# Kernel optimization log

Measured on AMD Instinct MI355X. Metric: run time of the kernel, lower is better.

## Reference

```python
import jax, jax.numpy as jnp
import numpy as np

# Multi-scale AvgPool3d pyramid (stride 1, zero padding, count_include_pad=True as in torch)
KERNELS = [(1, 1, 1), (1, 5, 5), (3, 13, 13), (5, 23, 23), (7, 31, 31), (9, 41, 41)]
WEIGHTS = [w / 100.0 for w in [20, 20, 20, 20, 20, 20, 10, 10]]
EPS = 1e-7  # BatchDiceLoss epsilon


def avgpool3d(x, k):
    # x: [B, C, D, H, W]; separable sum-pool per axis then divide by full kernel size
    # (equivalent to torch AvgPool3d with count_include_pad=True, stride 1, pad=(k-1)//2)
    y = x
    for axis, ks in zip((2, 3, 4), k):
        if ks > 1:
            window = [1] * 5
            window[axis] = ks
            pad = [(0, 0)] * 5
            pad[axis] = (ks // 2, ks // 2)
            y = jax.lax.reduce_window(y, 0.0, jax.lax.add, tuple(window), (1,) * 5, tuple(pad))
    return y / float(np.prod(k))


def batch_dice(pred, target):
    # BatchDiceLoss([1.0]): single label channel 0, flattened over the whole batch
    p = pred[:, 0].reshape(-1)
    t = target[:, 0].reshape(-1)
    inter = jnp.sum(p * t)
    return 1.0 - (2.0 * inter) / (jnp.sum(p) + jnp.sum(t) + EPS)


def multi_scale_dc(pred, target):
    loss = 0.0
    for k in KERNELS:
        pp = avgpool3d(avgpool3d(pred, k), k)   # pool applied twice per scale
        tt = avgpool3d(avgpool3d(target, k), k)
        loss = loss + batch_dice(pp, tt)
    return loss / len(KERNELS)


def setup_inputs() -> dict:
    key = jax.random.key(0)
    ks = jax.random.split(key, 14)
    vol = (4, 1, 28, 160, 160)
    u = lambda k: jax.random.uniform(k, vol, dtype=jnp.float32)
    return {
        "pr_core_c": u(ks[0]),
        "pr_core_p": u(ks[1]),
        "gt_core": u(ks[2]),
        "pr_lesion_c": u(ks[3]),
        "pr_lesion_p": u(ks[4]),
        "gt_lesion": u(ks[5]),
        "pr_penu_c": u(ks[6]),
        "pr_penu_p": u(ks[7]),
        "gt_penu": u(ks[8]),
        "output": jax.random.uniform(ks[9], (4, 6, 28, 160, 160), dtype=jnp.float32),
        "off_core_c": jax.random.normal(ks[10], (4, 3), dtype=jnp.float32),
        "off_penu_p": jax.random.normal(ks[11], (4, 3), dtype=jnp.float32),
        "off_target_c": jax.random.normal(ks[12], (4, 3), dtype=jnp.float32),
        "off_target_p": jax.random.normal(ks[13], (4, 3), dtype=jnp.float32),
    }


def reference(pr_core_c, pr_core_p, gt_core, pr_lesion_c, pr_lesion_p, gt_lesion,
              pr_penu_c, pr_penu_p, gt_penu, output,
              off_core_c, off_penu_p, off_target_c, off_target_p):
    loss = WEIGHTS[0] * multi_scale_dc(pr_core_c, gt_core)
    loss += WEIGHTS[1] * multi_scale_dc(pr_core_p, gt_core)
    loss += WEIGHTS[2] * multi_scale_dc(pr_lesion_c, gt_lesion)
    loss += WEIGHTS[3] * multi_scale_dc(pr_lesion_p, gt_lesion)
    loss += WEIGHTS[4] * multi_scale_dc(pr_penu_c, gt_penu)
    loss += WEIGHTS[5] * multi_scale_dc(pr_penu_p, gt_penu)
    # temporal monotonicity penalty: mean(|diff| - diff) per consecutive time pair
    diff = output[:, 1:] - output[:, :-1]           # [B, T-1, D, H, W]
    loss += WEIGHTS[6] * jnp.sum(jnp.mean(jnp.abs(diff) - diff, axis=(0, 2, 3, 4)))
    loss += WEIGHTS[7] * jnp.mean(jnp.abs(off_core_c - off_target_c))
    loss += WEIGHTS[7] * jnp.mean(jnp.abs(off_penu_p - off_target_p))
    return loss
```

## Files before the change

### kernel.cpp

```cpp
#include <hip/hip_runtime.h>
#include <hip/hip_fp16.h>


#define DIMB 4
#define DIMD 28
#define DIMH 160
#define DIMW 160
#define HW   (DIMH * DIMW)
#define DHW  (DIMD * HW)
#define VOL_N (DIMB * DHW)
#define PGRID 640
#define NSLOTS 91
#define DICE_EPS 1e-7
#define TBL_OFF (480 * 1024)

__device__ __forceinline__ float u2f(int pos, int k, int L) {
    if (k == 1) return 1.f;
    int r = k >> 1;
    float s = 0.f;
    for (int j = max(pos - r, 0); j <= min(pos + r, L - 1); ++j)
        s += (float)(min(j + r, L - 1) - max(j - r, 0) + 1);
    return s / (float)(k * k);
}

__device__ __forceinline__ float wave_sum(float v) {
#pragma unroll
    for (int o = 1; o < 64; o <<= 1) v += __shfl_xor(v, o, 64);
    return v;
}

__device__ __forceinline__ __half2 shfl_h2(__half2 v, int src) {
    int x = __shfl(*reinterpret_cast<int*>(&v), src, 64);
    return *reinterpret_cast<__half2*>(&x);
}

template<int K>
__device__ __forceinline__ void hstore(const float (&raw)[40],
                                       unsigned char* __restrict__ ob,
                                       int l, int c, int wl, int h0)
{
    constexpr int R = K / 2;
    constexpr float INVK = 1.f / (float)K;
    float ox[40];
#pragma unroll
    for (int i = 0; i < 40; ++i) ox[i] = raw[i];
#pragma unroll
    for (int pass = 0; pass < 4; ++pass) {
        float lo[R], hi[R];
#pragma unroll
        for (int i = 0; i < R; ++i) {
            float a = __shfl(ox[40 - R + i], l - 16, 64);
            lo[i] = (c == 0) ? 0.f : a;
            float b = __shfl(ox[i], l + 16, 64);
            hi[i] = (c == 3) ? 0.f : b;
        }
#define HWIN(j) ((j) < R ? lo[(j)] : ((j) < R + 40 ? ox[(j) - R] : hi[(j) - R - 40]))
        float out[40];
        float s = 0.f;
#pragma unroll
        for (int j = 0; j <= 2 * R; ++j) s += HWIN(j);
        out[0] = s * INVK;
#pragma unroll
        for (int i = 1; i < 40; ++i) {
            s += HWIN(i + 2 * R) - HWIN(i - 1);
            out[i] = s * INVK;
        }
#undef HWIN
#pragma unroll
        for (int i = 0; i < 40; ++i) ox[i] = out[i];
    }
#pragma unroll
    for (int i = 0; i < 40; ++i)
        ob[(h0 + i) * DIMW + wl] = (unsigned char)__float2uint_rn(ox[i] * 255.f);
}

__global__ __launch_bounds__(256) void hpool_tbl(const float* __restrict__ g0,
    const float* __restrict__ g1, const float* __restrict__ g2,
    unsigned char* __restrict__ bufs, float* __restrict__ tbl)
{
    int bx = blockIdx.x;
    if (bx < 840) {
        int u = bx * 2 + (threadIdx.x >> 7);
        int tt = threadIdx.x & 127;
        int g = u / 560, r = u - g * 560;
        int bd = r / 5, wt = r - bd * 5;
        const float* in = (g == 0) ? g0 : (g == 1) ? g1 : g2;
        int l = tt & 63, v = tt >> 6;
        int c = l >> 4, wl = v * 16 + (l & 15), h0 = c * 40;
        const float* base = in + (size_t)bd * HW + wt * 32;
        float raw[40];
#pragma unroll
        for (int i = 0; i < 40; ++i) raw[i] = base[(h0 + i) * DIMW + wl];
        unsigned char* ob = bufs + (size_t)g * 5 * VOL_N + (size_t)bd * HW + wt * 32;
        hstore<5> (raw, ob + 0 * (size_t)VOL_N, l, c, wl, h0);
        hstore<13>(raw, ob + 1 * (size_t)VOL_N, l, c, wl, h0);
        hstore<23>(raw, ob + 2 * (size_t)VOL_N, l, c, wl, h0);
        hstore<31>(raw, ob + 3 * (size_t)VOL_N, l, c, wl, h0);
        hstore<41>(raw, ob + 4 * (size_t)VOL_N, l, c, wl, h0);
    } else {
        const int KDa[6] = {1, 1, 3, 5, 7, 9};
        const int KHa[6] = {1, 5, 13, 23, 31, 41};
        for (int e = threadIdx.x; e < 1128; e += 256) {
            if (e < 960) tbl[e] = u2f(e % 160, KHa[e / 160], DIMH);
            else {
                int q = e - 960;
                tbl[e] = u2f(q % 28, KDa[q / 28], DIMD);
            }
        }
    }
}

template<int K, int KD>
__device__ __forceinline__ void wd_scale_pk(const unsigned char* __restrict__ tbA,
    const float4* __restrict__ c4, const float4* __restrict__ p4, int base4,
    unsigned int (*S)[164], float (*redS)[4], int t, int l, int wid, int rr,
    int c, bool act, double* __restrict__ partials, int slot_c, int slot_p,
    int bhA)
{
    constexpr int R = K / 2;
    const __half2 INVK2 = __float2half2_rn(1.f / (float)K);
    const __half2 Z2 = __float2half2_rn(0.f);
    __half2 ox[20];
    if (act) {
        unsigned int uA[5], uB[5];
#pragma unroll
        for (int q = 0; q < 5; ++q) {
            uA[q] = *(const unsigned int*)(tbA + 4 * q);
            uB[q] = *(const unsigned int*)(tbA + DIMW + 4 * q);
        }
#pragma unroll
        for (int q = 0; q < 5; ++q) {
#pragma unroll
            for (int j = 0; j < 4; ++j) {
                float fA = (float)((uA[q] >> (8 * j)) & 0xFFu);
                float fB = (float)((uB[q] >> (8 * j)) & 0xFFu);
                ox[4 * q + j] = __floats2half2_rn(fA, fB);
            }
        }
    } else {
#pragma unroll
        for (int i = 0; i < 20; ++i) ox[i] = Z2;
    }
#pragma unroll
    for (int pass = 0; pass < 4; ++pass) {
        __half2 lo[R], hi[R];
#pragma unroll
        for (int i = 0; i < R; ++i) {
            __half2 a = shfl_h2(ox[20 - R + i], l - 1);
            lo[i] = (c == 0) ? Z2 : a;
            __half2 b = shfl_h2(ox[i], l + 1);
            hi[i] = (c == 7) ? Z2 : b;
        }
#define WWIN(j) ((j) < R ? lo[(j)] : ((j) < R + 20 ? ox[(j) - R] : hi[(j) - R - 20]))
        __half2 out[20];
        __half2 s = Z2;
#pragma unroll
        for (int j = 0; j <= 2 * R; ++j) s = __hadd2(s, WWIN(j));
        out[0] = __hmul2(s, INVK2);
#pragma unroll
        for (int i = 1; i < 20; ++i) {
            s = __hadd2(s, __hsub2(WWIN(i + 2 * R), WWIN(i - 1)));
            out[i] = __hmul2(s, INVK2);
        }
#undef WWIN
#pragma unroll
        for (int i = 0; i < 20; ++i) ox[i] = out[i];
    }
    if (act) {
#pragma unroll
        for (int i = 0; i < 20; ++i)
            S[rr][c * 20 + i] = *reinterpret_cast<unsigned int*>(&ox[i]);
    }
    __syncthreads();
    if constexpr (KD > 1) {
        constexpr int RD = KD / 2;
        const __half2 INVKD2 = __float2half2_rn(1.f / (float)KD);
        if (t < DIMW) {
            __half2 x[28];
#pragma unroll
            for (int j = 0; j < 28; ++j)
                x[j] = *reinterpret_cast<const __half2*>(&S[j][t]);
#pragma unroll
            for (int p = 0; p < 4; ++p) {
                __half2 y[28];
                __half2 s = Z2;
#pragma unroll
                for (int j = 0; j <= RD; ++j) s = __hadd2(s, x[j]);
                y[0] = s;
#pragma unroll
                for (int i = 1; i < 28; ++i) {
                    if (i + RD < 28) s = __hadd2(s, x[i + RD]);
                    if (i - RD - 1 >= 0) s = __hsub2(s, x[i - RD - 1]);
                    y[i] = s;
                }
#pragma unroll
                for (int i = 0; i < 28; ++i) x[i] = __hmul2(y[i], INVKD2);
            }
#pragma unroll
            for (int j = 0; j < 28; ++j)
                S[j][t] = *reinterpret_cast<unsigned int*>(&x[j]);
        }
        __syncthreads();
    }
    float aicA = 0.f, aipA = 0.f, aicB = 0.f, aipB = 0.f;
    for (int e4 = t; e4 < 1120; e4 += 256) {
        int dd = e4 / 40, w4 = e4 - dd * 40;
        int fi = base4 + dd * (HW / 4) + w4;
        float4 vcA = c4[fi],      vpA = p4[fi];
        float4 vcB = c4[fi + 40], vpB = p4[fi + 40];
        const uint4 sv = *(const uint4*)&S[dd][4 * w4];
        float2 s0 = __half22float2(*reinterpret_cast<const __half2*>(&sv.x));
        float2 s1 = __half22float2(*reinterpret_cast<const __half2*>(&sv.y));
        float2 s2 = __half22float2(*reinterpret_cast<const __half2*>(&sv.z));
        float2 s3 = __half22float2(*reinterpret_cast<const __half2*>(&sv.w));
        aicA += vcA.x*s0.x + vcA.y*s1.x + vcA.z*s2.x + vcA.w*s3.x;
        aipA += vpA.x*s0.x + vpA.y*s1.x + vpA.z*s2.x + vpA.w*s3.x;
        aicB += vcB.x*s0.y + vcB.y*s1.y + vcB.z*s2.y + vcB.w*s3.y;
        aipB += vpB.x*s0.y + vpB.y*s1.y + vpB.z*s2.y + vpB.w*s3.y;
    }
    const float SC = 1.f / 255.f;
    float v0 = wave_sum(aicA) * SC, v1 = wave_sum(aipA) * SC;
    float v2 = wave_sum(aicB) * SC, v3 = wave_sum(aipB) * SC;
    if (l == 0) {
        redS[wid][0] = v0; redS[wid][1] = v1;
        redS[wid][2] = v2; redS[wid][3] = v3;
    }
    __syncthreads();
    if (t < 4) {
        double rv = (double)redS[0][t] + redS[1][t] + redS[2][t] + redS[3][t];
        int slot = (t & 1) ? slot_p : slot_c;
        int bh = bhA + (t >> 1);
        partials[(size_t)slot * PGRID + bh] = rv;
    }
}

__global__ __launch_bounds__(256) void wd_mix(const unsigned char* __restrict__ bufs,
    const float* __restrict__ pc0, const float* __restrict__ pp0,
    const float* __restrict__ pc1, const float* __restrict__ pp1,
    const float* __restrict__ pc2, const float* __restrict__ pp2,
    const float* __restrict__ tr0, const float* __restrict__ tr1,
    const float* __restrict__ tr2, const float* __restrict__ o6,
    const float* __restrict__ tbl, double* __restrict__ partials)
{
    __shared__ __align__(16) unsigned int S[DIMD][164];
    __shared__ float redS[4][24];
    int bx0 = blockIdx.x;
    int t = threadIdx.x;

    if (bx0 < 4800) {
        int w = (bx0 & 7) * 600 + (bx0 >> 3);
        int u = w / 5, q = w - u * 5;
        int g = u / 320, pj = u - g * 320;
        int bhA = 2 * pj;
        int b = bhA / DIMH, h = bhA - b * DIMH;
        const float* pc = (g == 0) ? pc0 : (g == 1) ? pc1 : pc2;
        const float* pp = (g == 0) ? pp0 : (g == 1) ? pp1 : pp2;
        size_t base0 = (size_t)b * DHW + (size_t)h * DIMW;
        int base4 = b * (DHW / 4) + h * 40;
        const float4* c4 = (const float4*)pc;
        const float4* p4 = (const float4*)pp;
        int l = t & 63, wid = t >> 6;
        int rr = wid * 7 + (l >> 3), c = l & 7;
        bool act = (l < 56);
        int sbuf = 4 - q;
        const unsigned char* tbA = bufs + (size_t)(g * 5 + sbuf) * VOL_N
                                 + base0 + (size_t)rr * HW + c * 20;
        int s = 5 - q;
        int slot_c = (2 * g) * 6 + s, slot_p = (2 * g + 1) * 6 + s;
        switch (q) {
            case 0: wd_scale_pk<41, 9>(tbA, c4, p4, base4, S, (float(*)[4])&redS[0][0], t, l, wid, rr, c, act, partials, slot_c, slot_p, bhA); break;
            case 1: wd_scale_pk<31, 7>(tbA, c4, p4, base4, S, (float(*)[4])&redS[0][0], t, l, wid, rr, c, act, partials, slot_c, slot_p, bhA); break;
            case 2: wd_scale_pk<23, 5>(tbA, c4, p4, base4, S, (float(*)[4])&redS[0][0], t, l, wid, rr, c, act, partials, slot_c, slot_p, bhA); break;
            case 3: wd_scale_pk<13, 3>(tbA, c4, p4, base4, S, (float(*)[4])&redS[0][0], t, l, wid, rr, c, act, partials, slot_c, slot_p, bhA); break;
            default: wd_scale_pk<5, 1>(tbA, c4, p4, base4, S, (float(*)[4])&redS[0][0], t, l, wid, rr, c, act, partials, slot_c, slot_p, bhA); break;
        }
        return;
    }

    if (bx0 < 6720) {
        int db = bx0 - 4800;
        int g = db / PGRID, blk = db - g * PGRID;
        const float* pc = (g == 0) ? pc0 : (g == 1) ? pc1 : pc2;
        const float* pp = (g == 0) ? pp0 : (g == 1) ? pp1 : pp2;
        const float* tr = (g == 0) ? tr0 : (g == 1) ? tr1 : tr2;
        const float4* c4p = (const float4*)pc;
        const float4* p4p = (const float4*)pp;
        const float4* t4p = (const float4*)tr;
        float vals[20];
#pragma unroll
        for (int i = 0; i < 20; ++i) vals[i] = 0.f;
        const int N4 = VOL_N / 4;
        for (int i4 = blk * 256 + t; i4 < N4; i4 += PGRID * 256) {
            int w4 = i4 % 40;
            int rest = i4 / 40;
            int h = rest % DIMH;
            int d = (rest / DIMH) % DIMD;
            float4 vc = c4p[i4], vp = p4p[i4], vt = t4p[i4];
            vals[0] += vc.x*vt.x + vc.y*vt.y + vc.z*vt.z + vc.w*vt.w;
            vals[1] += vp.x*vt.x + vp.y*vt.y + vp.z*vt.z + vp.w*vt.w;
#pragma unroll
            for (int s = 0; s < 6; ++s) {
                float cdh = tbl[960 + s * 28 + d] * tbl[s * 160 + h];
                const float4 cw = *(const float4*)(tbl + s * 160 + 4 * w4);
                vals[2 + s]  += cdh * (cw.x*vc.x + cw.y*vc.y + cw.z*vc.z + cw.w*vc.w);
                vals[8 + s]  += cdh * (cw.x*vp.x + cw.y*vp.y + cw.z*vp.z + cw.w*vp.w);
                vals[14 + s] += cdh * (cw.x*vt.x + cw.y*vt.y + cw.z*vt.z + cw.w*vt.w);
            }
        }
        int lane = t & 63, wid = t >> 6;
#pragma unroll
        for (int i = 0; i < 20; ++i) {
            float rv = wave_sum(vals[i]);
            if (lane == 0) redS[wid][i] = rv;
        }
        __syncthreads();
        if (t < 20) {
            double rv = (double)redS[0][t] + redS[1][t] + redS[2][t] + redS[3][t];
            int slot;
            if (t == 0) slot = (2 * g) * 6;
            else if (t == 1) slot = (2 * g + 1) * 6;
            else {
                int i = t - 2, vv = i / 6, s = i % 6;
                slot = (vv == 0) ? 36 + (2 * g) * 6 + s
                     : (vv == 1) ? 36 + (2 * g + 1) * 6 + s
                                 : 72 + g * 6 + s;
            }
            partials[(size_t)slot * PGRID + blk] = rv;
        }
        return;
    }

    int mb = bx0 - 6720;
    const int N4 = VOL_N / 4, PB = N4 / DIMB;
    float acc = 0.f;
    const float4* p = (const float4*)o6;
    for (int i = mb * 256 + t; i < N4; i += PGRID * 256) {
        int b = i / PB, r4 = i - b * PB;
        size_t a = (size_t)(b * 6) * PB + r4;
        float4 prev = p[a];
#pragma unroll
        for (int cc = 1; cc < 6; ++cc) {
            float4 cur = p[a + (size_t)cc * PB];
            acc += fmaxf(prev.x - cur.x, 0.f) + fmaxf(prev.y - cur.y, 0.f)
                 + fmaxf(prev.z - cur.z, 0.f) + fmaxf(prev.w - cur.w, 0.f);
            prev = cur;
        }
    }
    float rv = wave_sum(acc * 2.f);
    int lane = t & 63, wid = t >> 6;
    if (lane == 0) redS[wid][0] = rv;
    __syncthreads();
    if (t == 0)
        partials[(size_t)90 * PGRID + mb] =
            (double)redS[0][0] + redS[1][0] + redS[2][0] + redS[3][0];
}

__global__ __launch_bounds__(64) void fin_pre(const double* __restrict__ partials,
                                              double* __restrict__ ssum)
{
    int slot = blockIdx.x, t = threadIdx.x;
    double a = 0.0;
    for (int i = t; i < PGRID; i += 64) a += partials[(size_t)slot * PGRID + i];
#pragma unroll
    for (int o = 1; o < 64; o <<= 1) a += __shfl_xor(a, o, 64);
    if (t == 0) ssum[slot] = a;
}

__global__ void finalize(const double* __restrict__ ssum,
                         const float* __restrict__ off_a,
                         const float* __restrict__ off_b,
                         const float* __restrict__ off_ta,
                         const float* __restrict__ off_tb,
                         float* __restrict__ out)
{
    if (threadIdx.x == 0) {
        double loss = 0.0;
        for (int pair = 0; pair < 6; ++pair) {
            for (int s = 0; s < 6; ++s) {
                double inter = ssum[pair * 6 + s];
                double sp = ssum[36 + pair * 6 + s];
                double st = ssum[72 + (pair / 2) * 6 + s];
                loss += 0.2 * (1.0 - 2.0 * inter / (sp + st + DICE_EPS)) / 6.0;
            }
        }
        loss += 0.1 * (ssum[90] / (double)VOL_N);
        double oa = 0.0, ob = 0.0;
        for (int i = 0; i < 12; ++i) {
            oa += fabs((double)off_a[i] - (double)off_ta[i]);
            ob += fabs((double)off_b[i] - (double)off_tb[i]);
        }
        loss += 0.1 * (oa / 12.0) + 0.1 * (ob / 12.0);
        out[0] = (float)loss;
    }
}

extern "C" void kernel_launch(void* const* d_in, const int* in_sizes, int n_in,
                              void* d_out, int out_size, void* d_ws, size_t ws_size,
                              hipStream_t stream)
{
    double* partials = (double*)d_ws;
    double* ssum = partials + (size_t)NSLOTS * PGRID;
    float* tbl = (float*)((char*)d_ws + TBL_OFF);
    unsigned char* bufs = (unsigned char*)d_ws + 512 * 1024;

    const float* pred[6] = {(const float*)d_in[0], (const float*)d_in[1],
                            (const float*)d_in[3], (const float*)d_in[4],
                            (const float*)d_in[6], (const float*)d_in[7]};
    const float* gt[3] = {(const float*)d_in[2], (const float*)d_in[5],
                          (const float*)d_in[8]};

    hpool_tbl<<<841, 256, 0, stream>>>(gt[0], gt[1], gt[2], bufs, tbl);
    wd_mix<<<7360, 256, 0, stream>>>(bufs, pred[0], pred[1], pred[2], pred[3],
                                     pred[4], pred[5], gt[0], gt[1], gt[2],
                                     (const float*)d_in[9], tbl, partials);
    fin_pre<<<NSLOTS, 64, 0, stream>>>(partials, ssum);
    finalize<<<1, 64, 0, stream>>>(ssum,
                                   (const float*)d_in[10], (const float*)d_in[11],
                                   (const float*)d_in[12], (const float*)d_in[13],
                                   (float*)d_out);
}
```

Baseline: 114.5 us.

## Move dot-product and temporal-diff blocks into the prep kernel and re-layout byte buffers

The full-volume dot-product reductions and the temporal monotonicity reduction move from the second kernel into the first, so they run alongside the horizontal pooling pass. The coefficient table is now built per block in shared memory instead of global memory, and the heavy wd_mix kernel keeps only the pooling-scale blocks. The quantized byte buffers change layout from [b][d][h][w] to [b][h][d][w], so the 28 depth rows for one h are contiguous for the depth-pass loads. The trade-off is that every dot-product block recomputes the 1128-entry table and the store pattern in hstore becomes more strided.

```diff
diff --git a/kernel.cpp b/kernel.cpp
--- a/kernel.cpp
+++ b/kernel.cpp
@@ -9,10 +9,10 @@
 #define HW   (DIMH * DIMW)
 #define DHW  (DIMD * HW)
 #define VOL_N (DIMB * DHW)
+#define DW   (DIMD * DIMW)
 #define PGRID 640
 #define NSLOTS 91
 #define DICE_EPS 1e-7
-#define TBL_OFF (480 * 1024)
 
 __device__ __forceinline__ float u2f(int pos, int k, int L) {
     if (k == 1) return 1.f;
@@ -71,19 +71,28 @@
     }
 #pragma unroll
     for (int i = 0; i < 40; ++i)
-        ob[(h0 + i) * DIMW + wl] = (unsigned char)__float2uint_rn(ox[i] * 255.f);
-}
-
-__global__ __launch_bounds__(256) void hpool_tbl(const float* __restrict__ g0,
+        ob[(h0 + i) * DW + wl] = (unsigned char)__float2uint_rn(ox[i] * 255.f);
+}
+
+__global__ __launch_bounds__(256) void prep_mix(const float* __restrict__ g0,
     const float* __restrict__ g1, const float* __restrict__ g2,
-    unsigned char* __restrict__ bufs, float* __restrict__ tbl)
-{
+    const float* __restrict__ pc0, const float* __restrict__ pp0,
+    const float* __restrict__ pc1, const float* __restrict__ pp1,
+    const float* __restrict__ pc2, const float* __restrict__ pp2,
+    const float* __restrict__ o6, unsigned char* __restrict__ bufs,
+    double* __restrict__ partials)
+{
+    __shared__ __align__(16) float cT[1128];
+    __shared__ float redS[4][24];
     int bx = blockIdx.x;
+    int t = threadIdx.x;
+
     if (bx < 840) {
-        int u = bx * 2 + (threadIdx.x >> 7);
-        int tt = threadIdx.x & 127;
+        int u = bx * 2 + (t >> 7);
+        int tt = t & 127;
         int g = u / 560, r = u - g * 560;
         int bd = r / 5, wt = r - bd * 5;
+        int b = bd / DIMD, d = bd - b * DIMD;
         const float* in = (g == 0) ? g0 : (g == 1) ? g1 : g2;
         int l = tt & 63, v = tt >> 6;
         int c = l >> 4, wl = v * 16 + (l & 15), h0 = c * 40;
@@ -91,23 +100,102 @@
         float raw[40];
 #pragma unroll
         for (int i = 0; i < 40; ++i) raw[i] = base[(h0 + i) * DIMW + wl];
-        unsigned char* ob = bufs + (size_t)g * 5 * VOL_N + (size_t)bd * HW + wt * 32;
+        unsigned char* ob = bufs + (size_t)(g * 5) * VOL_N + (size_t)b * DHW
+                          + d * DIMW + wt * 32;
         hstore<5> (raw, ob + 0 * (size_t)VOL_N, l, c, wl, h0);
         hstore<13>(raw, ob + 1 * (size_t)VOL_N, l, c, wl, h0);
         hstore<23>(raw, ob + 2 * (size_t)VOL_N, l, c, wl, h0);
         hstore<31>(raw, ob + 3 * (size_t)VOL_N, l, c, wl, h0);
         hstore<41>(raw, ob + 4 * (size_t)VOL_N, l, c, wl, h0);
-    } else {
+        return;
+    }
+
+    if (bx < 2760) {
+        int db = bx - 840;
+        int g = db / PGRID, blk = db - g * PGRID;
         const int KDa[6] = {1, 1, 3, 5, 7, 9};
         const int KHa[6] = {1, 5, 13, 23, 31, 41};
-        for (int e = threadIdx.x; e < 1128; e += 256) {
-            if (e < 960) tbl[e] = u2f(e % 160, KHa[e / 160], DIMH);
+        for (int e = t; e < 1128; e += 256) {
+            if (e < 960) cT[e] = u2f(e % 160, KHa[e / 160], DIMH);
             else {
                 int q = e - 960;
-                tbl[e] = u2f(q % 28, KDa[q / 28], DIMD);
-            }
-        }
-    }
+                cT[e] = u2f(q % 28, KDa[q / 28], DIMD);
+            }
+        }
+        __syncthreads();
+        const float* pc = (g == 0) ? pc0 : (g == 1) ? pc1 : pc2;
+        const float* pp = (g == 0) ? pp0 : (g == 1) ? pp1 : pp2;
+        const float* tr = (g == 0) ? g0 : (g == 1) ? g1 : g2;
+        const float4* c4p = (const float4*)pc;
+        const float4* p4p = (const float4*)pp;
+        const float4* t4p = (const float4*)tr;
+        float vals[20];
+#pragma unroll
+        for (int i = 0; i < 20; ++i) vals[i] = 0.f;
+        const int N4 = VOL_N / 4;
+        for (int i4 = blk * 256 + t; i4 < N4; i4 += PGRID * 256) {
+            int w4 = i4 % 40;
+            int rest = i4 / 40;
+            int h = rest % DIMH;
+            int d = (rest / DIMH) % DIMD;
+            float4 vc = c4p[i4], vp = p4p[i4], vt = t4p[i4];
+            vals[0] += vc.x*vt.x + vc.y*vt.y + vc.z*vt.z + vc.w*vt.w;
+            vals[1] += vp.x*vt.x + vp.y*vt.y + vp.z*vt.z + vp.w*vt.w;
+#pragma unroll
+            for (int s = 0; s < 6; ++s) {
+                float cdh = cT[960 + s * 28 + d] * cT[s * 160 + h];
+                const float4 cw = *(const float4*)&cT[s * 160 + 4 * w4];
+                vals[2 + s]  += cdh * (cw.x*vc.x + cw.y*vc.y + cw.z*vc.z + cw.w*vc.w);
+                vals[8 + s]  += cdh * (cw.x*vp.x + cw.y*vp.y + cw.z*vp.z + cw.w*vp.w);
+                vals[14 + s] += cdh * (cw.x*vt.x + cw.y*vt.y + cw.z*vt.z + cw.w*vt.w);
+            }
+        }
+        int lane = t & 63, wid = t >> 6;
+#pragma unroll
+        for (int i = 0; i < 20; ++i) {
+            float rv = wave_sum(vals[i]);
+            if (lane == 0) redS[wid][i] = rv;
+        }
+        __syncthreads();
+        if (t < 20) {
+            double rv = (double)redS[0][t] + redS[1][t] + redS[2][t] + redS[3][t];
+            int slot;
+            if (t == 0) slot = (2 * g) * 6;
+            else if (t == 1) slot = (2 * g + 1) * 6;
+            else {
+                int i = t - 2, vv = i / 6, s = i % 6;
+                slot = (vv == 0) ? 36 + (2 * g) * 6 + s
+                     : (vv == 1) ? 36 + (2 * g + 1) * 6 + s
+                                 : 72 + g * 6 + s;
+            }
+            partials[(size_t)slot * PGRID + blk] = rv;
+        }
+        return;
+    }
+
+    int mb = bx - 2760;
+    const int N4 = VOL_N / 4, PB = N4 / DIMB;
+    float acc = 0.f;
+    const float4* p = (const float4*)o6;
+    for (int i = mb * 256 + t; i < N4; i += PGRID * 256) {
+        int b = i / PB, r4 = i - b * PB;
+        size_t a = (size_t)(b * 6) * PB + r4;
+        float4 prev = p[a];
+#pragma unroll
+        for (int cc = 1; cc < 6; ++cc) {
+            float4 cur = p[a + (size_t)cc * PB];
+            acc += fmaxf(prev.x - cur.x, 0.f) + fmaxf(prev.y - cur.y, 0.f)
+                 + fmaxf(prev.z - cur.z, 0.f) + fmaxf(prev.w - cur.w, 0.f);
+            prev = cur;
+        }
+    }
+    float rv = wave_sum(acc * 2.f);
+    int lane = t & 63, wid = t >> 6;
+    if (lane == 0) redS[wid][0] = rv;
+    __syncthreads();
+    if (t == 0)
+        partials[(size_t)90 * PGRID + mb] =
+            (double)redS[0][0] + redS[1][0] + redS[2][0] + redS[3][0];
 }
 
 template<int K, int KD>
@@ -126,7 +214,7 @@
 #pragma unroll
         for (int q = 0; q < 5; ++q) {
             uA[q] = *(const unsigned int*)(tbA + 4 * q);
-            uB[q] = *(const unsigned int*)(tbA + DIMW + 4 * q);
+            uB[q] = *(const unsigned int*)(tbA + DW + 4 * q);
         }
 #pragma unroll
         for (int q = 0; q < 5; ++q) {
@@ -238,121 +326,38 @@
     const float* __restrict__ pc0, const float* __restrict__ pp0,
     const float* __restrict__ pc1, const float* __restrict__ pp1,
     const float* __restrict__ pc2, const float* __restrict__ pp2,
-    const float* __restrict__ tr0, const float* __restrict__ tr1,
-    const float* __restrict__ tr2, const float* __restrict__ o6,
-    const float* __restrict__ tbl, double* __restrict__ partials)
+    double* __restrict__ partials)
 {
     __shared__ __align__(16) unsigned int S[DIMD][164];
     __shared__ float redS[4][24];
     int bx0 = blockIdx.x;
     int t = threadIdx.x;
-
-    if (bx0 < 4800) {
-        int w = (bx0 & 7) * 600 + (bx0 >> 3);
-        int u = w / 5, q = w - u * 5;
-        int g = u / 320, pj = u - g * 320;
-        int bhA = 2 * pj;
-        int b = bhA / DIMH, h = bhA - b * DIMH;
-        const float* pc = (g == 0) ? pc0 : (g == 1) ? pc1 : pc2;
-        const float* pp = (g == 0) ? pp0 : (g == 1) ? pp1 : pp2;
-        size_t base0 = (size_t)b * DHW + (size_t)h * DIMW;
-        int base4 = b * (DHW / 4) + h * 40;
-        const float4* c4 = (const float4*)pc;
-        const float4* p4 = (const float4*)pp;
-        int l = t & 63, wid = t >> 6;
-        int rr = wid * 7 + (l >> 3), c = l & 7;
-        bool act = (l < 56);
-        int sbuf = 4 - q;
-        const unsigned char* tbA = bufs + (size_t)(g * 5 + sbuf) * VOL_N
-                                 + base0 + (size_t)rr * HW + c * 20;
-        int s = 5 - q;
-        int slot_c = (2 * g) * 6 + s, slot_p = (2 * g + 1) * 6 + s;
-        switch (q) {
-            case 0: wd_scale_pk<41, 9>(tbA, c4, p4, base4, S, (float(*)[4])&redS[0][0], t, l, wid, rr, c, act, partials, slot_c, slot_p, bhA); break;
-            case 1: wd_scale_pk<31, 7>(tbA, c4, p4, base4, S, (float(*)[4])&redS[0][0], t, l, wid, rr, c, act, partials, slot_c, slot_p, bhA); break;
-            case 2: wd_scale_pk<23, 5>(tbA, c4, p4, base4, S, (float(*)[4])&redS[0][0], t, l, wid, rr, c, act, partials, slot_c, slot_p, bhA); break;
-            case 3: wd_scale_pk<13, 3>(tbA, c4, p4, base4, S, (float(*)[4])&redS[0][0], t, l, wid, rr, c, act, partials, slot_c, slot_p, bhA); break;
-            default: wd_scale_pk<5, 1>(tbA, c4, p4, base4, S, (float(*)[4])&redS[0][0], t, l, wid, rr, c, act, partials, slot_c, slot_p, bhA); break;
-        }
-        return;
-    }
-
-    if (bx0 < 6720) {
-        int db = bx0 - 4800;
-        int g = db / PGRID, blk = db - g * PGRID;
-        const float* pc = (g == 0) ? pc0 : (g == 1) ? pc1 : pc2;
-        const float* pp = (g == 0) ? pp0 : (g == 1) ? pp1 : pp2;
-        const float* tr = (g == 0) ? tr0 : (g == 1) ? tr1 : tr2;
-        const float4* c4p = (const float4*)pc;
-        const float4* p4p = (const float4*)pp;
-        const float4* t4p = (const float4*)tr;
-        float vals[20];
-#pragma unroll
-        for (int i = 0; i < 20; ++i) vals[i] = 0.f;
-        const int N4 = VOL_N / 4;
-        for (int i4 = blk * 256 + t; i4 < N4; i4 += PGRID * 256) {
-            int w4 = i4 % 40;
-            int rest = i4 / 40;
-            int h = rest % DIMH;
-            int d = (rest / DIMH) % DIMD;
-            float4 vc = c4p[i4], vp = p4p[i4], vt = t4p[i4];
-            vals[0] += vc.x*vt.x + vc.y*vt.y + vc.z*vt.z + vc.w*vt.w;
-            vals[1] += vp.x*vt.x + vp.y*vt.y + vp.z*vt.z + vp.w*vt.w;
-#pragma unroll
-            for (int s = 0; s < 6; ++s) {
-                float cdh = tbl[960 + s * 28 + d] * tbl[s * 160 + h];
-                const float4 cw = *(const float4*)(tbl + s * 160 + 4 * w4);
-                vals[2 + s]  += cdh * (cw.x*vc.x + cw.y*vc.y + cw.z*vc.z + cw.w*vc.w);
-                vals[8 + s]  += cdh * (cw.x*vp.x + cw.y*vp.y + cw.z*vp.z + cw.w*vp.w);
-                vals[14 + s] += cdh * (cw.x*vt.x + cw.y*vt.y + cw.z*vt.z + cw.w*vt.w);
-            }
-        }
-        int lane = t & 63, wid = t >> 6;
-#pragma unroll
-        for (int i = 0; i < 20; ++i) {
-            float rv = wave_sum(vals[i]);
-            if (lane == 0) redS[wid][i] = rv;
-        }
-        __syncthreads();
-        if (t < 20) {
-            double rv = (double)redS[0][t] + redS[1][t] + redS[2][t] + redS[3][t];
-            int slot;
-            if (t == 0) slot = (2 * g) * 6;
-            else if (t == 1) slot = (2 * g + 1) * 6;
-            else {
-                int i = t - 2, vv = i / 6, s = i % 6;
-                slot = (vv == 0) ? 36 + (2 * g) * 6 + s
-                     : (vv == 1) ? 36 + (2 * g + 1) * 6 + s
-                                 : 72 + g * 6 + s;
-            }
-            partials[(size_t)slot * PGRID + blk] = rv;
-        }
-        return;
-    }
-
-    int mb = bx0 - 6720;
-    const int N4 = VOL_N / 4, PB = N4 / DIMB;
-    float acc = 0.f;
-    const float4* p = (const float4*)o6;
-    for (int i = mb * 256 + t; i < N4; i += PGRID * 256) {
-        int b = i / PB, r4 = i - b * PB;
-        size_t a = (size_t)(b * 6) * PB + r4;
-        float4 prev = p[a];
-#pragma unroll
-        for (int cc = 1; cc < 6; ++cc) {
-            float4 cur = p[a + (size_t)cc * PB];
-            acc += fmaxf(prev.x - cur.x, 0.f) + fmaxf(prev.y - cur.y, 0.f)
-                 + fmaxf(prev.z - cur.z, 0.f) + fmaxf(prev.w - cur.w, 0.f);
-            prev = cur;
-        }
-    }
-    float rv = wave_sum(acc * 2.f);
-    int lane = t & 63, wid = t >> 6;
-    if (lane == 0) redS[wid][0] = rv;
-    __syncthreads();
-    if (t == 0)
-        partials[(size_t)90 * PGRID + mb] =
-            (double)redS[0][0] + redS[1][0] + redS[2][0] + redS[3][0];
+    int w = (bx0 & 7) * 600 + (bx0 >> 3);
+    int u = w / 5, q = w - u * 5;
+    int g = u / 320, pj = u - g * 320;
+    int bhA = 2 * pj;
+    int b = bhA / DIMH, h = bhA - b * DIMH;
+    const float* pc = (g == 0) ? pc0 : (g == 1) ? pc1 : pc2;
+    const float* pp = (g == 0) ? pp0 : (g == 1) ? pp1 : pp2;
+    int base4 = b * (DHW / 4) + h * 40;
+    const float4* c4 = (const float4*)pc;
+    const float4* p4 = (const float4*)pp;
+    int l = t & 63, wid = t >> 6;
+    int rr = wid * 7 + (l >> 3), c = l & 7;
+    bool act = (l < 56);
+    int sbuf = 4 - q;
+    const unsigned char* tbA = bufs + (size_t)(g * 5 + sbuf) * VOL_N
+                             + (size_t)b * DHW + (size_t)h * DW
+                             + rr * DIMW + c * 20;
+    int s = 5 - q;
+    int slot_c = (2 * g) * 6 + s, slot_p = (2 * g + 1) * 6 + s;
+    switch (q) {
+        case 0: wd_scale_pk<41, 9>(tbA, c4, p4, base4, S, (float(*)[4])&redS[0][0], t, l, wid, rr, c, act, partials, slot_c, slot_p, bhA); break;
+        case 1: wd_scale_pk<31, 7>(tbA, c4, p4, base4, S, (float(*)[4])&redS[0][0], t, l, wid, rr, c, act, partials, slot_c, slot_p, bhA); break;
+        case 2: wd_scale_pk<23, 5>(tbA, c4, p4, base4, S, (float(*)[4])&redS[0][0], t, l, wid, rr, c, act, partials, slot_c, slot_p, bhA); break;
+        case 3: wd_scale_pk<13, 3>(tbA, c4, p4, base4, S, (float(*)[4])&redS[0][0], t, l, wid, rr, c, act, partials, slot_c, slot_p, bhA); break;
+        default: wd_scale_pk<5, 1>(tbA, c4, p4, base4, S, (float(*)[4])&redS[0][0], t, l, wid, rr, c, act, partials, slot_c, slot_p, bhA); break;
+    }
 }
 
 __global__ __launch_bounds__(64) void fin_pre(const double* __restrict__ partials,
@@ -400,7 +405,6 @@
 {
     double* partials = (double*)d_ws;
     double* ssum = partials + (size_t)NSLOTS * PGRID;
-    float* tbl = (float*)((char*)d_ws + TBL_OFF);
     unsigned char* bufs = (unsigned char*)d_ws + 512 * 1024;
 
     const float* pred[6] = {(const float*)d_in[0], (const float*)d_in[1],
@@ -409,10 +413,12 @@
     const float* gt[3] = {(const float*)d_in[2], (const float*)d_in[5],
                           (const float*)d_in[8]};
 
-    hpool_tbl<<<841, 256, 0, stream>>>(gt[0], gt[1], gt[2], bufs, tbl);
-    wd_mix<<<7360, 256, 0, stream>>>(bufs, pred[0], pred[1], pred[2], pred[3],
-                                     pred[4], pred[5], gt[0], gt[1], gt[2],
-                                     (const float*)d_in[9], tbl, partials);
+    prep_mix<<<3400, 256, 0, stream>>>(gt[0], gt[1], gt[2],
+                                       pred[0], pred[1], pred[2], pred[3],
+                                       pred[4], pred[5],
+                                       (const float*)d_in[9], bufs, partials);
+    wd_mix<<<4800, 256, 0, stream>>>(bufs, pred[0], pred[1], pred[2], pred[3],
+                                     pred[4], pred[5], partials);
     fin_pre<<<NSLOTS, 64, 0, stream>>>(partials, ssum);
     finalize<<<1, 64, 0, stream>>>(ssum,
                                    (const float*)d_in[10], (const float*)d_in[11],
```

After: 140.7 us. +22.9%, slower.
